# Optimization experiments

Measured on AMD Instinct MI355X. Metric: run time of the kernel, lower is better.

The kernel has to match this reference:

```python
import jax, jax.numpy as jnp
import numpy as np

HIDDEN = 1024
Q_OUT = 2048
KV_OUT = 1024
HEAD_DIM = 128
N_Q = Q_OUT // HEAD_DIM      # 16
N_KV = KV_OUT // HEAD_DIM    # 8
EPS = 1e-6
ROPE_BASE = 10000.0


def _rms_norm(x, w, eps=EPS):
    # normalize over last dim (head_dim)
    ms = jnp.mean(x * x, axis=-1, keepdims=True)
    return x * jax.lax.rsqrt(ms + eps) * w


def _rope_cos_sin(t, dim=HEAD_DIM, base=ROPE_BASE):
    inv_freq = 1.0 / (base ** (jnp.arange(0, dim, 2, dtype=jnp.float32) / dim))
    pos = jnp.arange(t, dtype=jnp.float32)
    freqs = pos[:, None] * inv_freq[None, :]          # (T, D/2)
    emb = jnp.concatenate([freqs, freqs], axis=-1)    # (T, D)
    return jnp.cos(emb), jnp.sin(emb)


def _rotate_half(x):
    d = x.shape[-1] // 2
    return jnp.concatenate([-x[..., d:], x[..., :d]], axis=-1)


def setup_inputs() -> dict:
    key = jax.random.key(0)
    ks = jax.random.split(key, 7)
    def lin(k, fan_in, fan_out):
        # nn.Linear default init: U(-1/sqrt(fan_in), 1/sqrt(fan_in)); stored as (in, out) for x @ W
        bound = 1.0 / np.sqrt(fan_in)
        return jax.random.uniform(k, (fan_in, fan_out), jnp.float32, -bound, bound)
    return {
        "x": jax.random.normal(ks[0], (2, 2048, HIDDEN), jnp.float32),
        "Wq": lin(ks[1], HIDDEN, Q_OUT),
        "Wk": lin(ks[2], HIDDEN, KV_OUT),
        "Wv": lin(ks[3], HIDDEN, KV_OUT),
        "Wo": lin(ks[4], Q_OUT, HIDDEN),
        "q_norm_w": jnp.ones((HEAD_DIM,), jnp.float32),
        "k_norm_w": jnp.ones((HEAD_DIM,), jnp.float32),
    }


def reference(x, Wq, Wk, Wv, Wo, q_norm_w, k_norm_w):
    b, t, _ = x.shape
    # QKV projections, shaped to (B, H, T, D)
    q = (x @ Wq).reshape(b, t, N_Q, HEAD_DIM).transpose(0, 2, 1, 3)
    k = (x @ Wk).reshape(b, t, N_KV, HEAD_DIM).transpose(0, 2, 1, 3)
    v = (x @ Wv).reshape(b, t, N_KV, HEAD_DIM).transpose(0, 2, 1, 3)
    # per-head RMSNorm on q/k
    q = _rms_norm(q, q_norm_w)
    k = _rms_norm(k, k_norm_w)
    # RoPE (positions 0..T-1)
    cos, sin = _rope_cos_sin(t)                        # (T, D)
    cos = cos[None, None]; sin = sin[None, None]       # (1,1,T,D)
    q = q * cos + _rotate_half(q) * sin
    k = k * cos + _rotate_half(k) * sin
    # GQA: repeat_interleave kv heads to match q heads
    rep = N_Q // N_KV
    k_r = jnp.repeat(k, rep, axis=1)                   # (B, Hq, T, D)
    v_r = jnp.repeat(v, rep, axis=1)
    # causal attention
    scores = jnp.einsum('bhqd,bhkd->bhqk', q, k_r) / jnp.sqrt(jnp.asarray(HEAD_DIM, x.dtype))
    causal = jnp.triu(jnp.full((t, t), -jnp.inf, dtype=scores.dtype), k=1)[None, None]
    attn = jax.nn.softmax(scores + causal, axis=-1)
    out = jnp.einsum('bhqk,bhkd->bhqd', attn, v_r)     # (B, Hq, T, D)
    out = out.transpose(0, 2, 1, 3).reshape(b, t, Q_OUT)
    return out @ Wo
```

## Files before the change

### kernel.cpp

```cpp
#include <hip/hip_runtime.h>
#include <math.h>

typedef __attribute__((ext_vector_type(8))) short short8;
typedef __attribute__((ext_vector_type(4))) float f32x4;
typedef __attribute__((ext_vector_type(4))) unsigned int uint4v;

#define HIDDEN 1024
#define QOUT 2048
#define KVOUT 1024
#define HD 128
#define TSEQ 2048

__device__ __forceinline__ float bf2f(unsigned short h) {
    union { unsigned int u; float f; } x; x.u = ((unsigned int)h) << 16; return x.f;
}
__device__ __forceinline__ unsigned short f2bf(float f) {
    union { float f; unsigned int u; } x; x.f = f;
    unsigned int r = (x.u + 0x7fffu + ((x.u >> 16) & 1u)) >> 16;
    return (unsigned short)r;
}
__device__ __forceinline__ unsigned int cvtpk(float lo, float hi) {
    unsigned int r;
    asm("v_cvt_pk_bf16_f32 %0, %1, %2" : "=v"(r) : "v"(lo), "v"(hi));
    return r;
}

__device__ __forceinline__ void glds16(const unsigned short* g, unsigned short* l) {
    __builtin_amdgcn_global_load_lds(
        (const __attribute__((address_space(1))) unsigned int*)g,
        (__attribute__((address_space(3))) unsigned int*)l, 16, 0, 0);
}

__global__ __launch_bounds__(256) void prep(const float* __restrict__ x,
                                            const float* __restrict__ Wq,
                                            const float* __restrict__ Wk,
                                            const float* __restrict__ Wv,
                                            const float* __restrict__ Wo,
                                            unsigned short* __restrict__ xb,
                                            unsigned short* __restrict__ Wt,
                                            unsigned short* __restrict__ Wot) {
    int bid = blockIdx.x;
    int tid = threadIdx.x;
    if (bid < 4096) {
        int i = bid * 256 + tid;
        float4 v = *(const float4*)(x + (size_t)i * 4);
        unsigned short o[4] = {f2bf(v.x), f2bf(v.y), f2bf(v.z), f2bf(v.w)};
        *(unsigned long long*)(xb + (size_t)i * 4) = *(unsigned long long*)o;
        return;
    }
    bid -= 4096;
    const float* W; unsigned short* D; int K, N;
    if (bid < 512)       { W = Wq; D = Wt;                          K = 1024; N = 2048; }
    else if (bid < 768)  { bid -= 512;  W = Wk; D = Wt + (size_t)2048 * 1024; K = 1024; N = 1024; }
    else if (bid < 1024) { bid -= 768;  W = Wv; D = Wt + (size_t)3072 * 1024; K = 1024; N = 1024; }
    else                 { bid -= 1024; W = Wo; D = Wot;                      K = 2048; N = 1024; }
    __shared__ __attribute__((aligned(16))) unsigned short Ls[64 * 72];
    int ntiles = N >> 6;
    int kt = bid / ntiles, nt = bid - kt * ntiles;
    int k0 = kt * 64, n0 = nt * 64;
    for (int t = 0; t < 4; t++) {
        int idx = tid + t * 256;
        int r = idx >> 4, seg = idx & 15;
        float4 v = *(const float4*)(W + (size_t)(k0 + r) * N + n0 + seg * 4);
        int c = seg * 4;
        Ls[(c + 0) * 72 + r] = f2bf(v.x);
        Ls[(c + 1) * 72 + r] = f2bf(v.y);
        Ls[(c + 2) * 72 + r] = f2bf(v.z);
        Ls[(c + 3) * 72 + r] = f2bf(v.w);
    }
    __syncthreads();
    for (int t = 0; t < 2; t++) {
        int idx = tid + t * 256;
        int rr = idx >> 3, seg = idx & 7;
        uint4v v = *(const uint4v*)(Ls + rr * 72 + seg * 8);
        *(uint4v*)(D + (size_t)(n0 + rr) * K + k0 + seg * 8) = v;
    }
}

template <int OUT_BF16, int BN>
__global__ __launch_bounds__(256) void gemm_bt(const unsigned short* __restrict__ A,
                                               const unsigned short* __restrict__ Bt,
                                               void* __restrict__ Cout,
                                               int M, int N, int K) {
    constexpr int MT = (BN == 128) ? 4 : 2;
    __shared__ __attribute__((aligned(16))) unsigned short As[2][128 * 32];
    __shared__ __attribute__((aligned(16))) unsigned short Bs[2][BN * 32];
    const int tid = threadIdx.x;
    const int lane = tid & 63;
    const int warp = tid >> 6;
    const int ln = lane & 15;
    const int quad = lane >> 4;
    const int wm = (BN == 128) ? (warp >> 1) : warp;
    const int wn = (BN == 128) ? (warp & 1) : 0;
    const int m0 = blockIdx.y * 128;
    const int n0 = blockIdx.x * BN;

    const int srow = lane >> 2;
    const int schunk = (lane & 3) ^ (srow & 3);
    const unsigned short* Ag = A + (size_t)(m0 + warp * 16 + srow) * K + schunk * 8;
    const unsigned short* Bg = Bt + (size_t)(n0 + warp * 16 + srow) * K + schunk * 8;

    f32x4 acc[MT][4];
#pragma unroll
    for (int i = 0; i < MT; i++)
#pragma unroll
        for (int j = 0; j < 4; j++) acc[i][j] = (f32x4){0.f, 0.f, 0.f, 0.f};

    auto stage = [&](int k0, int bi) {
        glds16(Ag + k0, As[bi] + warp * 16 * 32);
        glds16(Ag + (size_t)64 * K + k0, As[bi] + warp * 16 * 32 + 64 * 32);
        glds16(Bg + k0, Bs[bi] + warp * 16 * 32);
        if (BN == 128) glds16(Bg + (size_t)64 * K + k0, Bs[bi] + warp * 16 * 32 + 64 * 32);
    };

    const int rq = quad ^ (ln & 3);
    const int KI = K >> 5;
    stage(0, 0);
    for (int it = 0; it < KI; it++) {
        __syncthreads();
        if (it + 1 < KI) stage((it + 1) << 5, (it + 1) & 1);
        const unsigned short* Ab = As[it & 1];
        const unsigned short* Bb = Bs[it & 1];
        short8 af[MT], bf[4];
#pragma unroll
        for (int mt = 0; mt < MT; mt++)
            af[mt] = *(const short8*)(Ab + (wm * (MT * 16) + mt * 16 + ln) * 32 + rq * 8);
#pragma unroll
        for (int nt = 0; nt < 4; nt++)
            bf[nt] = *(const short8*)(Bb + (wn * 64 + nt * 16 + ln) * 32 + rq * 8);
#pragma unroll
        for (int mt = 0; mt < MT; mt++)
#pragma unroll
            for (int nt = 0; nt < 4; nt++)
                acc[mt][nt] = __builtin_amdgcn_mfma_f32_16x16x32_bf16(bf[nt], af[mt], acc[mt][nt], 0, 0, 0);
    }
#pragma unroll
    for (int mt = 0; mt < MT; mt++) {
        int row = m0 + wm * (MT * 16) + mt * 16 + ln;
#pragma unroll
        for (int nt = 0; nt < 4; nt++) {
            int colb = n0 + wn * 64 + nt * 16 + quad * 4;
            if (OUT_BF16) {
                unsigned long long pk =
                    (unsigned long long)cvtpk(acc[mt][nt][0], acc[mt][nt][1]) |
                    ((unsigned long long)cvtpk(acc[mt][nt][2], acc[mt][nt][3]) << 32);
                *(unsigned long long*)((unsigned short*)Cout + (size_t)row * N + colb) = pk;
            } else {
                *(f32x4*)((float*)Cout + (size_t)row * N + colb) = acc[mt][nt];
            }
        }
    }
}

__global__ __launch_bounds__(256) void gemm_o(const unsigned short* __restrict__ A,
                                              const unsigned short* __restrict__ Bt,
                                              float* __restrict__ Cout,
                                              int M, int N, int K) {
    __shared__ __attribute__((aligned(16))) unsigned short As[2][128 * 64];
    __shared__ __attribute__((aligned(16))) unsigned short Bs[2][64 * 64];
    const int tid = threadIdx.x;
    const int lane = tid & 63;
    const int warp = tid >> 6;
    const int ln = lane & 15;
    const int quad = lane >> 4;
    const int m0 = blockIdx.y * 128;
    const int n0 = blockIdx.x * 64;

    const int srow = lane >> 3;
    const int schunk = (lane & 7) ^ srow;
    const unsigned short* Ag = A + (size_t)(m0 + warp * 32 + srow) * K + schunk * 8;
    const unsigned short* Bg = Bt + (size_t)(n0 + warp * 16 + srow) * K + schunk * 8;

    f32x4 acc[2][4];
#pragma unroll
    for (int i = 0; i < 2; i++)
#pragma unroll
        for (int j = 0; j < 4; j++) acc[i][j] = (f32x4){0.f, 0.f, 0.f, 0.f};

    auto stage = [&](int k0, int bi) {
#pragma unroll
        for (int g = 0; g < 4; g++)
            glds16(Ag + (size_t)(g * 8) * K + k0, As[bi] + (warp * 32 + g * 8) * 64);
#pragma unroll
        for (int g = 0; g < 2; g++)
            glds16(Bg + (size_t)(g * 8) * K + k0, Bs[bi] + (warp * 16 + g * 8) * 64);
    };

    const int KI = K >> 6;
    stage(0, 0);
    for (int it = 0; it < KI; it++) {
        __syncthreads();
        if (it + 1 < KI) stage((it + 1) << 6, (it + 1) & 1);
        const unsigned short* Ab = As[it & 1];
        const unsigned short* Bb = Bs[it & 1];
#pragma unroll
        for (int ks = 0; ks < 2; ks++) {
            const int rc = ((ks << 2) + quad) ^ (ln & 7);
            short8 af[2], bf[4];
#pragma unroll
            for (int mt = 0; mt < 2; mt++)
                af[mt] = *(const short8*)(Ab + (warp * 32 + mt * 16 + ln) * 64 + rc * 8);
#pragma unroll
            for (int nt = 0; nt < 4; nt++)
                bf[nt] = *(const short8*)(Bb + (nt * 16 + ln) * 64 + rc * 8);
#pragma unroll
            for (int mt = 0; mt < 2; mt++)
#pragma unroll
                for (int nt = 0; nt < 4; nt++)
                    acc[mt][nt] = __builtin_amdgcn_mfma_f32_16x16x32_bf16(bf[nt], af[mt], acc[mt][nt], 0, 0, 0);
        }
    }
#pragma unroll
    for (int mt = 0; mt < 2; mt++) {
        int row = m0 + warp * 32 + mt * 16 + ln;
#pragma unroll
        for (int nt = 0; nt < 4; nt++) {
            int colb = n0 + nt * 16 + quad * 4;
            *(f32x4*)(Cout + (size_t)row * N + colb) = acc[mt][nt];
        }
    }
}

__global__ __launch_bounds__(256) void nrvt(const unsigned short* __restrict__ QKV,
                                            const float* __restrict__ qw,
                                            const float* __restrict__ kw,
                                            unsigned short* __restrict__ Q,
                                            unsigned short* __restrict__ Kb,
                                            unsigned short* __restrict__ Vt) {
    if (blockIdx.x < 12288) {
        const int tid = threadIdx.x;
        const int l5 = tid & 31;
        const int task = blockIdx.x * 8 + (tid >> 5);
        const int tok = task / 24;
        const int slot = task - tok * 24;
        const int b = tok >> 11, t = tok & 2047;
        const float* w;
        unsigned short* dst;
        int col0;
        float sc;
        if (slot < 16) {
            col0 = slot * HD;
            dst = Q + ((size_t)(b * 16 + slot) * TSEQ + t) * HD;
            w = qw;
            sc = 0.12750580997495268f;
        } else {
            int hk = slot - 16;
            col0 = QOUT + hk * HD;
            dst = Kb + ((size_t)(b * 8 + hk) * TSEQ + t) * HD;
            w = kw;
            sc = 1.0f;
        }
        const unsigned short* row = QKV + (size_t)tok * 4096 + col0;
        unsigned long long pkin = *(const unsigned long long*)(row + l5 * 4);
        unsigned short us[4];
        *(unsigned long long*)us = pkin;
        float e[4];
        float ss = 0.f;
#pragma unroll
        for (int k = 0; k < 4; k++) { e[k] = bf2f(us[k]); ss += e[k] * e[k]; }
#pragma unroll
        for (int off = 1; off < 32; off <<= 1) ss += __shfl_xor(ss, off);
        float rr = rsqrtf(ss * (1.0f / 128.0f) + 1e-6f);
        float4 wv = *(const float4*)(w + l5 * 4);
        float n[4] = { e[0] * rr * wv.x, e[1] * rr * wv.y, e[2] * rr * wv.z, e[3] * rr * wv.w };
        float np[4];
#pragma unroll
        for (int k = 0; k < 4; k++) np[k] = __shfl_xor(n[k], 16);
        const float tf = (float)t;
        const int fb = (l5 & 15) * 4;
        const bool hi = (l5 >= 16);
        unsigned short outs[4];
#pragma unroll
        for (int k = 0; k < 4; k++) {
            float invf = __builtin_exp2f(-(float)(fb + k) * 0.20762050593045951f);
            float sf, cf;
            __sincosf(tf * invf, &sf, &cf);
            float o = hi ? (n[k] * cf + np[k] * sf) : (n[k] * cf - np[k] * sf);
            outs[k] = f2bf(o * sc);
        }
        *(unsigned long long*)(dst + l5 * 4) = *(unsigned long long*)outs;
        return;
    }
    __shared__ __attribute__((aligned(16))) unsigned short Ls[128 * 72];
    int bid = blockIdx.x - 12288;
    int tt = bid & 31, hk = (bid >> 5) & 7, b = bid >> 8;
    int t0 = tt * 64;
    int tid = threadIdx.x;
    const unsigned short* base = QKV + (size_t)(b * 2048 + t0) * 4096 + 3072 + hk * 128;
    for (int i = 0; i < 4; i++) {
        int idx = tid + i * 256;
        int r = idx >> 4, seg = idx & 15;
        uint4v v = *(const uint4v*)(base + (size_t)r * 4096 + seg * 8);
        unsigned short* pv = (unsigned short*)&v;
        int d = seg * 8;
        for (int jj = 0; jj < 8; jj++) Ls[(d + jj) * 72 + r] = pv[jj];
    }
    __syncthreads();
    unsigned short* out = Vt + (size_t)(b * 8 + hk) * 128 * 2048;
    for (int i = 0; i < 4; i++) {
        int idx = tid + i * 256;
        int d = idx >> 3, seg = idx & 7;
        uint4v v = *(const uint4v*)(Ls + d * 72 + seg * 8);
        *(uint4v*)(out + (size_t)d * 2048 + t0 + seg * 8) = v;
    }
}

__global__ __launch_bounds__(256, 2) void attn(const unsigned short* __restrict__ Q,
                                               const unsigned short* __restrict__ Kg,
                                               const unsigned short* __restrict__ Vt,
                                               unsigned short* __restrict__ Og) {
    __shared__ __attribute__((aligned(16))) unsigned short Ks[2][64 * 128];
    __shared__ __attribute__((aligned(16))) unsigned short Vs[2][128 * 64];
    __shared__ __attribute__((aligned(16))) unsigned short Ps[4][16 * 72];
    const int p = blockIdx.x;
    const int bh = blockIdx.y;
    const int b = bh >> 4, h = bh & 15, hk = h >> 1;
    const int tid = threadIdx.x;
    const int warp = tid >> 6, lane = tid & 63, ln = lane & 15, quad = lane >> 4;
    const int strip[2] = { p * 64 + warp * 16, (31 - p) * 64 + warp * 16 };
    const int jdiag[2] = { p, 31 - p };

    const unsigned short* Kbase = Kg + (size_t)(b * 8 + hk) * TSEQ * HD;
    const unsigned short* Vbase = Vt + (size_t)(b * 8 + hk) * HD * TSEQ;
    const unsigned short* Qh = Q + (size_t)(b * 16 + h) * TSEQ * HD;

    short8 qf[2][4];
#pragma unroll
    for (int st = 0; st < 2; st++)
#pragma unroll
        for (int kt = 0; kt < 4; kt++)
            qf[st][kt] = *(const short8*)(Qh + (size_t)(strip[st] + ln) * HD + kt * 32 + quad * 8);

    f32x4 o[2][8];
    f32x4 lac[2];
#pragma unroll
    for (int st = 0; st < 2; st++) {
        lac[st] = (f32x4){0.f, 0.f, 0.f, 0.f};
#pragma unroll
        for (int ot = 0; ot < 8; ot++) o[st][ot] = (f32x4){0.f, 0.f, 0.f, 0.f};
    }
    float m_[2] = {-1e30f, -1e30f};

    const int kr = lane >> 4;
    const int kc = lane & 15;
    const int vr = lane >> 3;
    const int vc = lane & 7;

    auto stage_kv = [&](int jt, int bi) {
        const int j0s = jt * 64;
        unsigned short* KsB = Ks[bi];
        unsigned short* VsB = Vs[bi];
#pragma unroll
        for (int c = 0; c < 4; c++) {
            int row = warp * 16 + c * 4 + kr;
            glds16(Kbase + (size_t)(j0s + row) * HD + ((kc ^ (row & 15)) * 8),
                   KsB + (warp * 16 + c * 4) * 128);
        }
#pragma unroll
        for (int c = 0; c < 4; c++) {
            int d = warp * 32 + c * 8 + vr;
            glds16(Vbase + (size_t)d * TSEQ + j0s + ((vc ^ (d & 7)) * 8),
                   VsB + (warp * 32 + c * 8) * 64);
        }
    };

    short8 ones8;
#pragma unroll
    for (int i = 0; i < 8; i++) ones8[i] = (short)0x3F80;

    const int nT = 32 - p;
    stage_kv(0, 0);
    for (int j = 0; j < nT; j++) {
        __syncthreads();
        if (j + 1 < nT) stage_kv(j + 1, (j + 1) & 1);
        const unsigned short* KsC = Ks[j & 1];
        const unsigned short* VsC = Vs[j & 1];
        const bool act0 = (j <= jdiag[0]);
        f32x4 s[2][4];
#pragma unroll
        for (int kb = 0; kb < 4; kb++) {
            s[0][kb] = (f32x4){0.f, 0.f, 0.f, 0.f};
            s[1][kb] = (f32x4){0.f, 0.f, 0.f, 0.f};
        }
        __builtin_amdgcn_s_setprio(1);
#pragma unroll
        for (int kt = 0; kt < 4; kt++) {
            short8 kf[4];
#pragma unroll
            for (int kb = 0; kb < 4; kb++)
                kf[kb] = *(const short8*)(KsC + (kb * 16 + ln) * 128 + (((kt * 4 + quad) ^ ln) * 8));
#pragma unroll
            for (int kb = 0; kb < 4; kb++)
                s[1][kb] = __builtin_amdgcn_mfma_f32_16x16x32_bf16(kf[kb], qf[1][kt], s[1][kb], 0, 0, 0);
            if (act0)
#pragma unroll
                for (int kb = 0; kb < 4; kb++)
                    s[0][kb] = __builtin_amdgcn_mfma_f32_16x16x32_bf16(kf[kb], qf[0][kt], s[0][kb], 0, 0, 0);
        }
        __builtin_amdgcn_s_setprio(0);
        short8 pf[2][2];
        bool needR[2] = {false, false};
        float alpha[2] = {1.f, 1.f};
#pragma unroll
        for (int st = 0; st < 2; st++) {
            if (st == 0 && !act0) continue;
            float mk[4];
            if (j == jdiag[st]) {
                const int qloc = warp * 16 + ln;
#pragma unroll
                for (int kb = 0; kb < 4; kb++) {
#pragma unroll
                    for (int r = 0; r < 4; r++) {
                        int kvloc = kb * 16 + quad * 4 + r;
                        if (kvloc > qloc) s[st][kb][r] = -1e30f;
                    }
                    mk[kb] = fmaxf(fmaxf(s[st][kb][0], s[st][kb][1]),
                                   fmaxf(s[st][kb][2], s[st][kb][3]));
                }
            } else {
#pragma unroll
                for (int kb = 0; kb < 4; kb++)
                    mk[kb] = fmaxf(fmaxf(s[st][kb][0], s[st][kb][1]),
                                   fmaxf(s[st][kb][2], s[st][kb][3]));
            }
            float mx = fmaxf(fmaxf(mk[0], mk[1]), fmaxf(mk[2], mk[3]));
            float mn = m_[st];
            if (!__all(mx <= mn + 8.0f)) {
                mx = fmaxf(mx, __shfl_xor(mx, 16));
                mx = fmaxf(mx, __shfl_xor(mx, 32));
                mn = fmaxf(m_[st], mx);
                alpha[st] = __builtin_exp2f(m_[st] - mn);
                m_[st] = mn;
                needR[st] = true;
            }
#pragma unroll
            for (int kb = 0; kb < 4; kb++) {
                float p0 = __builtin_exp2f(s[st][kb][0] - mn);
                float p1 = __builtin_exp2f(s[st][kb][1] - mn);
                float p2 = __builtin_exp2f(s[st][kb][2] - mn);
                float p3 = __builtin_exp2f(s[st][kb][3] - mn);
                unsigned long long pk =
                    (unsigned long long)cvtpk(p0, p1) |
                    ((unsigned long long)cvtpk(p2, p3) << 32);
                *(unsigned long long*)(&Ps[warp][ln * 72 + kb * 16 + quad * 4]) = pk;
            }
            pf[st][0] = *(const short8*)(&Ps[warp][ln * 72 + quad * 8]);
            pf[st][1] = *(const short8*)(&Ps[warp][ln * 72 + 32 + quad * 8]);
        }
        if (act0 && needR[0]) {
            float a = alpha[0];
#pragma unroll
            for (int ot = 0; ot < 8; ot++)
#pragma unroll
                for (int r = 0; r < 4; r++) o[0][ot][r] *= a;
#pragma unroll
            for (int r = 0; r < 4; r++) lac[0][r] *= a;
        }
        if (needR[1]) {
            float a = alpha[1];
#pragma unroll
            for (int ot = 0; ot < 8; ot++)
#pragma unroll
                for (int r = 0; r < 4; r++) o[1][ot][r] *= a;
#pragma unroll
            for (int r = 0; r < 4; r++) lac[1][r] *= a;
        }
        __builtin_amdgcn_s_setprio(1);
        lac[1] = __builtin_amdgcn_mfma_f32_16x16x32_bf16(ones8, pf[1][0], lac[1], 0, 0, 0);
        lac[1] = __builtin_amdgcn_mfma_f32_16x16x32_bf16(ones8, pf[1][1], lac[1], 0, 0, 0);
        if (act0) {
            lac[0] = __builtin_amdgcn_mfma_f32_16x16x32_bf16(ones8, pf[0][0], lac[0], 0, 0, 0);
            lac[0] = __builtin_amdgcn_mfma_f32_16x16x32_bf16(ones8, pf[0][1], lac[0], 0, 0, 0);
        }
#pragma unroll
        for (int ot = 0; ot < 8; ot++) {
            short8 vf0 = *(const short8*)(VsC + (ot * 16 + ln) * 64 + ((quad ^ (ln & 7)) * 8));
            short8 vf1 = *(const short8*)(VsC + (ot * 16 + ln) * 64 + (((4 + quad) ^ (ln & 7)) * 8));
            o[1][ot] = __builtin_amdgcn_mfma_f32_16x16x32_bf16(vf0, pf[1][0], o[1][ot], 0, 0, 0);
            o[1][ot] = __builtin_amdgcn_mfma_f32_16x16x32_bf16(vf1, pf[1][1], o[1][ot], 0, 0, 0);
            if (act0) {
                o[0][ot] = __builtin_amdgcn_mfma_f32_16x16x32_bf16(vf0, pf[0][0], o[0][ot], 0, 0, 0);
                o[0][ot] = __builtin_amdgcn_mfma_f32_16x16x32_bf16(vf1, pf[0][1], o[0][ot], 0, 0, 0);
            }
        }
        __builtin_amdgcn_s_setprio(0);
    }
#pragma unroll
    for (int st = 0; st < 2; st++) {
        float inv = 1.0f / lac[st][0];
        size_t rowoff = ((size_t)(b * TSEQ + strip[st] + ln)) * QOUT + h * 128 + quad * 4;
#pragma unroll
        for (int ot = 0; ot < 8; ot++) {
            unsigned long long pk =
                (unsigned long long)cvtpk(o[st][ot][0] * inv, o[st][ot][1] * inv) |
                ((unsigned long long)cvtpk(o[st][ot][2] * inv, o[st][ot][3] * inv) << 32);
            *(unsigned long long*)(Og + rowoff + ot * 16) = pk;
        }
    }
}

extern "C" void kernel_launch(void* const* d_in, const int* in_sizes, int n_in,
                              void* d_out, int out_size, void* d_ws, size_t ws_size,
                              hipStream_t stream) {
    (void)in_sizes; (void)n_in; (void)out_size;
    const float* x  = (const float*)d_in[0];
    const float* Wq = (const float*)d_in[1];
    const float* Wk = (const float*)d_in[2];
    const float* Wv = (const float*)d_in[3];
    const float* Wo = (const float*)d_in[4];
    const float* qw = (const float*)d_in[5];
    const float* kw = (const float*)d_in[6];

    char* ws = (char*)d_ws;
    const size_t MB = 1024 * 1024;
    unsigned short* Wt   = (unsigned short*)(ws);
    unsigned short* Wot  = (unsigned short*)(ws + 8 * MB);
    unsigned short* QKVb = (unsigned short*)(ws + 12 * MB);
    unsigned short* xb   = (unsigned short*)(ws + 44 * MB);
    unsigned short* Qb   = (unsigned short*)(ws + 52 * MB);
    unsigned short* Kb   = (unsigned short*)(ws + 68 * MB);
    unsigned short* Vtb  = (unsigned short*)(ws + 76 * MB);
    unsigned short* Ob   = (unsigned short*)(ws + 84 * MB);
    if (ws_size < 100 * MB) return;

    prep<<<dim3(5632), 256, 0, stream>>>(x, Wq, Wk, Wv, Wo, xb, Wt, Wot);
    gemm_bt<1, 128><<<dim3(32, 32), 256, 0, stream>>>(xb, Wt, QKVb, 4096, 4096, 1024);
    nrvt<<<dim3(12800), 256, 0, stream>>>(QKVb, qw, kw, Qb, Kb, Vtb);
    attn<<<dim3(16, 32), 256, 0, stream>>>(Qb, Kb, Vtb, Ob);
    gemm_o<<<dim3(16, 32), 256, 0, stream>>>(Ob, Wot, (float*)d_out, 4096, 1024, 2048);
}
```

Baseline: 261.1 us.

## Split attention strip pair across 8 warps instead of 2 strips per warp

```diff
diff --git a/kernel.cpp b/kernel.cpp
--- a/kernel.cpp
+++ b/kernel.cpp
@@ -305,41 +305,38 @@
     }
 }
 
-__global__ __launch_bounds__(256, 2) void attn(const unsigned short* __restrict__ Q,
+__global__ __launch_bounds__(512, 4) void attn(const unsigned short* __restrict__ Q,
                                                const unsigned short* __restrict__ Kg,
                                                const unsigned short* __restrict__ Vt,
                                                unsigned short* __restrict__ Og) {
     __shared__ __attribute__((aligned(16))) unsigned short Ks[2][64 * 128];
     __shared__ __attribute__((aligned(16))) unsigned short Vs[2][128 * 64];
-    __shared__ __attribute__((aligned(16))) unsigned short Ps[4][16 * 72];
+    __shared__ __attribute__((aligned(16))) unsigned short Ps[8][8][16][8];
     const int p = blockIdx.x;
     const int bh = blockIdx.y;
     const int b = bh >> 4, h = bh & 15, hk = h >> 1;
     const int tid = threadIdx.x;
-    const int warp = tid >> 6, lane = tid & 63, ln = lane & 15, quad = lane >> 4;
-    const int strip[2] = { p * 64 + warp * 16, (31 - p) * 64 + warp * 16 };
-    const int jdiag[2] = { p, 31 - p };
+    const int w = tid >> 6, lane = tid & 63, ln = lane & 15, quad = lane >> 4;
+    const int sg = w >> 2;
+    const int wi = w & 3;
+    const int tile = sg ? (31 - p) : p;
+    const int jdiag = tile;
+    const int qrow0 = tile * 64 + wi * 16;
 
     const unsigned short* Kbase = Kg + (size_t)(b * 8 + hk) * TSEQ * HD;
     const unsigned short* Vbase = Vt + (size_t)(b * 8 + hk) * HD * TSEQ;
     const unsigned short* Qh = Q + (size_t)(b * 16 + h) * TSEQ * HD;
 
-    short8 qf[2][4];
-#pragma unroll
-    for (int st = 0; st < 2; st++)
-#pragma unroll
-        for (int kt = 0; kt < 4; kt++)
-            qf[st][kt] = *(const short8*)(Qh + (size_t)(strip[st] + ln) * HD + kt * 32 + quad * 8);
-
-    f32x4 o[2][8];
-    f32x4 lac[2];
-#pragma unroll
-    for (int st = 0; st < 2; st++) {
-        lac[st] = (f32x4){0.f, 0.f, 0.f, 0.f};
-#pragma unroll
-        for (int ot = 0; ot < 8; ot++) o[st][ot] = (f32x4){0.f, 0.f, 0.f, 0.f};
-    }
-    float m_[2] = {-1e30f, -1e30f};
+    short8 qf[4];
+#pragma unroll
+    for (int kt = 0; kt < 4; kt++)
+        qf[kt] = *(const short8*)(Qh + (size_t)(qrow0 + ln) * HD + kt * 32 + quad * 8);
+
+    f32x4 o[8];
+    f32x4 lac = (f32x4){0.f, 0.f, 0.f, 0.f};
+#pragma unroll
+    for (int ot = 0; ot < 8; ot++) o[ot] = (f32x4){0.f, 0.f, 0.f, 0.f};
+    float m_ = -1e30f;
 
     const int kr = lane >> 4;
     const int kc = lane & 15;
@@ -351,16 +348,16 @@
         unsigned short* KsB = Ks[bi];
         unsigned short* VsB = Vs[bi];
 #pragma unroll
-        for (int c = 0; c < 4; c++) {
-            int row = warp * 16 + c * 4 + kr;
+        for (int c = 0; c < 2; c++) {
+            int row = w * 8 + c * 4 + kr;
             glds16(Kbase + (size_t)(j0s + row) * HD + ((kc ^ (row & 15)) * 8),
-                   KsB + (warp * 16 + c * 4) * 128);
-        }
-#pragma unroll
-        for (int c = 0; c < 4; c++) {
-            int d = warp * 32 + c * 8 + vr;
+                   KsB + (w * 8 + c * 4) * 128);
+        }
+#pragma unroll
+        for (int c = 0; c < 2; c++) {
+            int d = w * 16 + c * 8 + vr;
             glds16(Vbase + (size_t)d * TSEQ + j0s + ((vc ^ (d & 7)) * 8),
-                   VsB + (warp * 32 + c * 8) * 64);
+                   VsB + (w * 16 + c * 8) * 64);
         }
     };
 
@@ -368,6 +365,7 @@
 #pragma unroll
     for (int i = 0; i < 8; i++) ones8[i] = (short)0x3F80;
 
+    unsigned short* Pw = &Ps[w][0][0][0];
     const int nT = 32 - p;
     stage_kv(0, 0);
     for (int j = 0; j < nT; j++) {
@@ -375,127 +373,94 @@
         if (j + 1 < nT) stage_kv(j + 1, (j + 1) & 1);
         const unsigned short* KsC = Ks[j & 1];
         const unsigned short* VsC = Vs[j & 1];
-        const bool act0 = (j <= jdiag[0]);
-        f32x4 s[2][4];
-#pragma unroll
-        for (int kb = 0; kb < 4; kb++) {
-            s[0][kb] = (f32x4){0.f, 0.f, 0.f, 0.f};
-            s[1][kb] = (f32x4){0.f, 0.f, 0.f, 0.f};
-        }
-        __builtin_amdgcn_s_setprio(1);
-#pragma unroll
-        for (int kt = 0; kt < 4; kt++) {
-            short8 kf[4];
-#pragma unroll
-            for (int kb = 0; kb < 4; kb++)
-                kf[kb] = *(const short8*)(KsC + (kb * 16 + ln) * 128 + (((kt * 4 + quad) ^ ln) * 8));
-#pragma unroll
-            for (int kb = 0; kb < 4; kb++)
-                s[1][kb] = __builtin_amdgcn_mfma_f32_16x16x32_bf16(kf[kb], qf[1][kt], s[1][kb], 0, 0, 0);
-            if (act0)
+        const bool act = sg ? true : (j <= jdiag);
+        if (act) {
+            f32x4 s[4];
+#pragma unroll
+            for (int kb = 0; kb < 4; kb++) s[kb] = (f32x4){0.f, 0.f, 0.f, 0.f};
+            __builtin_amdgcn_s_setprio(1);
+#pragma unroll
+            for (int kt = 0; kt < 4; kt++) {
+                short8 kf[4];
 #pragma unroll
                 for (int kb = 0; kb < 4; kb++)
-                    s[0][kb] = __builtin_amdgcn_mfma_f32_16x16x32_bf16(kf[kb], qf[0][kt], s[0][kb], 0, 0, 0);
-        }
-        __builtin_amdgcn_s_setprio(0);
-        short8 pf[2][2];
-        bool needR[2] = {false, false};
-        float alpha[2] = {1.f, 1.f};
-#pragma unroll
-        for (int st = 0; st < 2; st++) {
-            if (st == 0 && !act0) continue;
+                    kf[kb] = *(const short8*)(KsC + (kb * 16 + ln) * 128 + (((kt * 4 + quad) ^ ln) * 8));
+#pragma unroll
+                for (int kb = 0; kb < 4; kb++)
+                    s[kb] = __builtin_amdgcn_mfma_f32_16x16x32_bf16(kf[kb], qf[kt], s[kb], 0, 0, 0);
+            }
+            __builtin_amdgcn_s_setprio(0);
             float mk[4];
-            if (j == jdiag[st]) {
-                const int qloc = warp * 16 + ln;
+            if (j == jdiag) {
+                const int qloc = wi * 16 + ln;
 #pragma unroll
                 for (int kb = 0; kb < 4; kb++) {
 #pragma unroll
                     for (int r = 0; r < 4; r++) {
                         int kvloc = kb * 16 + quad * 4 + r;
-                        if (kvloc > qloc) s[st][kb][r] = -1e30f;
+                        if (kvloc > qloc) s[kb][r] = -1e30f;
                     }
-                    mk[kb] = fmaxf(fmaxf(s[st][kb][0], s[st][kb][1]),
-                                   fmaxf(s[st][kb][2], s[st][kb][3]));
+                    mk[kb] = fmaxf(fmaxf(s[kb][0], s[kb][1]), fmaxf(s[kb][2], s[kb][3]));
                 }
             } else {
 #pragma unroll
                 for (int kb = 0; kb < 4; kb++)
-                    mk[kb] = fmaxf(fmaxf(s[st][kb][0], s[st][kb][1]),
-                                   fmaxf(s[st][kb][2], s[st][kb][3]));
+                    mk[kb] = fmaxf(fmaxf(s[kb][0], s[kb][1]), fmaxf(s[kb][2], s[kb][3]));
             }
             float mx = fmaxf(fmaxf(mk[0], mk[1]), fmaxf(mk[2], mk[3]));
-            float mn = m_[st];
+            float mn = m_;
+            bool needR = false;
+            float alpha = 1.f;
             if (!__all(mx <= mn + 8.0f)) {
                 mx = fmaxf(mx, __shfl_xor(mx, 16));
                 mx = fmaxf(mx, __shfl_xor(mx, 32));
-                mn = fmaxf(m_[st], mx);
-                alpha[st] = __builtin_exp2f(m_[st] - mn);
-                m_[st] = mn;
-                needR[st] = true;
+                mn = fmaxf(m_, mx);
+                alpha = __builtin_exp2f(m_ - mn);
+                m_ = mn;
+                needR = true;
             }
 #pragma unroll
             for (int kb = 0; kb < 4; kb++) {
-                float p0 = __builtin_exp2f(s[st][kb][0] - mn);
-                float p1 = __builtin_exp2f(s[st][kb][1] - mn);
-                float p2 = __builtin_exp2f(s[st][kb][2] - mn);
-                float p3 = __builtin_exp2f(s[st][kb][3] - mn);
+                float p0 = __builtin_exp2f(s[kb][0] - mn);
+                float p1 = __builtin_exp2f(s[kb][1] - mn);
+                float p2 = __builtin_exp2f(s[kb][2] - mn);
+                float p3 = __builtin_exp2f(s[kb][3] - mn);
                 unsigned long long pk =
                     (unsigned long long)cvtpk(p0, p1) |
                     ((unsigned long long)cvtpk(p2, p3) << 32);
-                *(unsigned long long*)(&Ps[warp][ln * 72 + kb * 16 + quad * 4]) = pk;
-            }
-            pf[st][0] = *(const short8*)(&Ps[warp][ln * 72 + quad * 8]);
-            pf[st][1] = *(const short8*)(&Ps[warp][ln * 72 + 32 + quad * 8]);
-        }
-        if (act0 && needR[0]) {
-            float a = alpha[0];
-#pragma unroll
-            for (int ot = 0; ot < 8; ot++)
-#pragma unroll
-                for (int r = 0; r < 4; r++) o[0][ot][r] *= a;
-#pragma unroll
-            for (int r = 0; r < 4; r++) lac[0][r] *= a;
-        }
-        if (needR[1]) {
-            float a = alpha[1];
-#pragma unroll
-            for (int ot = 0; ot < 8; ot++)
-#pragma unroll
-                for (int r = 0; r < 4; r++) o[1][ot][r] *= a;
-#pragma unroll
-            for (int r = 0; r < 4; r++) lac[1][r] *= a;
-        }
-        __builtin_amdgcn_s_setprio(1);
-        lac[1] = __builtin_amdgcn_mfma_f32_16x16x32_bf16(ones8, pf[1][0], lac[1], 0, 0, 0);
-        lac[1] = __builtin_amdgcn_mfma_f32_16x16x32_bf16(ones8, pf[1][1], lac[1], 0, 0, 0);
-        if (act0) {
-            lac[0] = __builtin_amdgcn_mfma_f32_16x16x32_bf16(ones8, pf[0][0], lac[0], 0, 0, 0);
-            lac[0] = __builtin_amdgcn_mfma_f32_16x16x32_bf16(ones8, pf[0][1], lac[0], 0, 0, 0);
-        }
-#pragma unroll
-        for (int ot = 0; ot < 8; ot++) {
-            short8 vf0 = *(const short8*)(VsC + (ot * 16 + ln) * 64 + ((quad ^ (ln & 7)) * 8));
-            short8 vf1 = *(const short8*)(VsC + (ot * 16 + ln) * 64 + (((4 + quad) ^ (ln & 7)) * 8));
-            o[1][ot] = __builtin_amdgcn_mfma_f32_16x16x32_bf16(vf0, pf[1][0], o[1][ot], 0, 0, 0);
-            o[1][ot] = __builtin_amdgcn_mfma_f32_16x16x32_bf16(vf1, pf[1][1], o[1][ot], 0, 0, 0);
-            if (act0) {
-                o[0][ot] = __builtin_amdgcn_mfma_f32_16x16x32_bf16(vf0, pf[0][0], o[0][ot], 0, 0, 0);
-                o[0][ot] = __builtin_amdgcn_mfma_f32_16x16x32_bf16(vf1, pf[0][1], o[0][ot], 0, 0, 0);
-            }
-        }
-        __builtin_amdgcn_s_setprio(0);
-    }
-#pragma unroll
-    for (int st = 0; st < 2; st++) {
-        float inv = 1.0f / lac[st][0];
-        size_t rowoff = ((size_t)(b * TSEQ + strip[st] + ln)) * QOUT + h * 128 + quad * 4;
-#pragma unroll
-        for (int ot = 0; ot < 8; ot++) {
-            unsigned long long pk =
-                (unsigned long long)cvtpk(o[st][ot][0] * inv, o[st][ot][1] * inv) |
-                ((unsigned long long)cvtpk(o[st][ot][2] * inv, o[st][ot][3] * inv) << 32);
-            *(unsigned long long*)(Og + rowoff + ot * 16) = pk;
-        }
+                *(unsigned long long*)(Pw + (2 * kb + (quad >> 1)) * 128 + ln * 8 + (quad & 1) * 4) = pk;
+            }
+            short8 pf0 = *(const short8*)(Pw + quad * 128 + ln * 8);
+            short8 pf1 = *(const short8*)(Pw + (4 + quad) * 128 + ln * 8);
+            if (needR) {
+#pragma unroll
+                for (int ot = 0; ot < 8; ot++)
+#pragma unroll
+                    for (int r = 0; r < 4; r++) o[ot][r] *= alpha;
+#pragma unroll
+                for (int r = 0; r < 4; r++) lac[r] *= alpha;
+            }
+            __builtin_amdgcn_s_setprio(1);
+            lac = __builtin_amdgcn_mfma_f32_16x16x32_bf16(ones8, pf0, lac, 0, 0, 0);
+            lac = __builtin_amdgcn_mfma_f32_16x16x32_bf16(ones8, pf1, lac, 0, 0, 0);
+#pragma unroll
+            for (int ot = 0; ot < 8; ot++) {
+                short8 vf0 = *(const short8*)(VsC + (ot * 16 + ln) * 64 + ((quad ^ (ln & 7)) * 8));
+                short8 vf1 = *(const short8*)(VsC + (ot * 16 + ln) * 64 + (((4 + quad) ^ (ln & 7)) * 8));
+                o[ot] = __builtin_amdgcn_mfma_f32_16x16x32_bf16(vf0, pf0, o[ot], 0, 0, 0);
+                o[ot] = __builtin_amdgcn_mfma_f32_16x16x32_bf16(vf1, pf1, o[ot], 0, 0, 0);
+            }
+            __builtin_amdgcn_s_setprio(0);
+        }
+    }
+    float inv = 1.0f / lac[0];
+    size_t rowoff = ((size_t)(b * TSEQ + qrow0 + ln)) * QOUT + h * 128 + quad * 4;
+#pragma unroll
+    for (int ot = 0; ot < 8; ot++) {
+        unsigned long long pk =
+            (unsigned long long)cvtpk(o[ot][0] * inv, o[ot][1] * inv) |
+            ((unsigned long long)cvtpk(o[ot][2] * inv, o[ot][3] * inv) << 32);
+        *(unsigned long long*)(Og + rowoff + ot * 16) = pk;
     }
 }
 
@@ -526,6 +491,6 @@
     prep<<<dim3(5632), 256, 0, stream>>>(x, Wq, Wk, Wv, Wo, xb, Wt, Wot);
     gemm_bt<1, 128><<<dim3(32, 32), 256, 0, stream>>>(xb, Wt, QKVb, 4096, 4096, 1024);
     nrvt<<<dim3(12800), 256, 0, stream>>>(QKVb, qw, kw, Qb, Kb, Vtb);
-    attn<<<dim3(16, 32), 256, 0, stream>>>(Qb, Kb, Vtb, Ob);
+    attn<<<dim3(16, 32), 512, 0, stream>>>(Qb, Kb, Vtb, Ob);
     gemm_o<<<dim3(16, 32), 256, 0, stream>>>(Ob, Wot, (float*)d_out, 4096, 1024, 2048);
 }
```

Result: faster. 249.2 us (-4.6%).
